# Optimization experiments

Measured on AMD Instinct MI355X. Metric: run time of the kernel, lower is better.

Reference implementation:

```python
import jax, jax.numpy as jnp
import numpy as np

DEPTH = 4
DIM = 128
M_DIM = 16
FEAT_DIM = 10
K = 12
CLAMP = 2.0
B, N = 4, 2048
EI = 2 * DIM + 1  # edge_input_dim = feats_i + feats_j + rel_dist


def setup_inputs() -> dict:
    key = jax.random.key(0)
    ks = jax.random.split(key, 16)
    def p(k, shape, s=0.05):
        return jax.random.normal(k, shape, dtype=jnp.float32) * s
    inp = dict(
        feats=jax.random.normal(ks[0], (B, N, FEAT_DIM), dtype=jnp.float32),
        coords=jax.random.normal(ks[1], (B, N, 3), dtype=jnp.float32) * 3.0,
        mask=jnp.ones((B, N), dtype=bool),
        emb_w=p(ks[2], (FEAT_DIM, DIM)), emb_b=p(ks[3], (DIM,)),
        ew1=p(ks[4], (DEPTH, EI, 2 * EI)), eb1=p(ks[5], (DEPTH, 2 * EI)),
        ew2=p(ks[6], (DEPTH, 2 * EI, M_DIM)), eb2=p(ks[7], (DEPTH, M_DIM)),
        cw1=p(ks[8], (DEPTH, M_DIM, 4 * M_DIM)), cb1=p(ks[9], (DEPTH, 4 * M_DIM)),
        cw2=p(ks[10], (DEPTH, 4 * M_DIM, 1)), cb2=p(ks[11], (DEPTH, 1)),
        cscale=jnp.full((DEPTH, 1), 1e-2, dtype=jnp.float32),  # CoorsNorm scale_init
        nw1=p(ks[12], (DEPTH, DIM + M_DIM, 2 * DIM)), nb1=p(ks[13], (DEPTH, 2 * DIM)),
        nw2=p(ks[14], (DEPTH, 2 * DIM, DIM)), nb2=p(ks[15], (DEPTH, DIM)),
    )
    return inp


def _egnn_layer(feats, coors, mask, lp):
    ew1, eb1, ew2, eb2, cw1, cb1, cw2, cb2, cscale, nw1, nb1, nw2, nb2 = lp
    # pairwise relative coords / squared distances
    rel = coors[:, :, None, :] - coors[:, None, :, :]            # (B,N,N,3)
    dist = jnp.sum(rel * rel, axis=-1)                           # (B,N,N)
    pm = mask[:, :, None] & mask[:, None, :]
    ranking = jnp.where(pm, dist, 1e5)
    _, nbhd = jax.lax.top_k(-ranking, K)                         # (B,N,K) smallest dists
    rel_k = jnp.take_along_axis(rel, nbhd[..., None], axis=2)    # (B,N,K,3)
    dist_k = jnp.take_along_axis(dist, nbhd, axis=2)             # (B,N,K)
    feats_j = jax.vmap(lambda f, i: f[i])(feats, nbhd)           # (B,N,K,D)
    mask_j = jnp.take_along_axis(jnp.broadcast_to(mask[:, None, :], dist.shape), nbhd, axis=2)
    m2 = mask[:, :, None] & mask_j                               # (B,N,K)
    feats_i = jnp.broadcast_to(feats[:, :, None, :], feats_j.shape)
    edge_in = jnp.concatenate([feats_i, feats_j, dist_k[..., None]], axis=-1)  # (B,N,K,EI)
    m_ij = jax.nn.silu(jax.nn.silu(edge_in @ ew1 + eb1) @ ew2 + eb2)           # (B,N,K,M)
    # coordinate update (E(n)-equivariant)
    w = (jax.nn.silu(m_ij @ cw1 + cb1) @ cw2 + cb2)[..., 0]      # (B,N,K)
    nrm = jnp.sqrt(jnp.sum(rel_k * rel_k, axis=-1, keepdims=True))
    rel_n = rel_k / jnp.maximum(nrm, 1e-8) * cscale              # CoorsNorm
    w = jnp.clip(jnp.where(m2, w, 0.0), -CLAMP, CLAMP)
    coors_out = coors + jnp.einsum('bik,bikc->bic', w, rel_n)
    # node update (residual)
    m_i = jnp.sum(jnp.where(m2[..., None], m_ij, 0.0), axis=2)   # (B,N,M)
    node_in = jnp.concatenate([feats, m_i], axis=-1)
    feats_out = jax.nn.silu(node_in @ nw1 + nb1) @ nw2 + nb2 + feats
    return feats_out, coors_out


def reference(feats, coords, mask, emb_w, emb_b, ew1, eb1, ew2, eb2, cw1, cb1, cw2, cb2, cscale, nw1, nb1, nw2, nb2):
    h = feats @ emb_w + emb_b                                    # continuous feature embedding
    c = coords
    for l in range(DEPTH):
        lp = (ew1[l], eb1[l], ew2[l], eb2[l], cw1[l], cb1[l], cw2[l], cb2[l],
              cscale[l], nw1[l], nb1[l], nw2[l], nb2[l])
        h, c = _egnn_layer(h, c, mask, lp)
    mf = mask.astype(h.dtype)
    out = jnp.sum(h * mf[..., None], axis=1) / jnp.sum(mf, axis=1, keepdims=True)  # (B,DIM)
    return out
```

## Files before the change

kernel.cpp:

```cpp
#include <hip/hip_runtime.h>
#include <hip/hip_bf16.h>
#include <math.h>

#define NB 4
#define NN 2048
#define DIMF 128
#define MD 16
#define KK 12
#define NODES (NB*NN)

typedef __attribute__((ext_vector_type(8))) short bf16x8;
typedef __attribute__((ext_vector_type(4))) float f32x4;

__device__ __forceinline__ float silu_f(float x) {
    return x * __builtin_amdgcn_rcpf(1.0f + __expf(-x));
}

__device__ __forceinline__ short f2bf(float x) {
    unsigned u = __float_as_uint(x);
    unsigned r = (u + 0x7FFFu + ((u >> 16) & 1u)) >> 16;
    return (short)r;
}

__device__ __forceinline__ short2 pkbf(float a, float b) {
    union { __hip_bfloat162 h; short2 s; } u;
    u.h = __float22bfloat162_rn(make_float2(a, b));
    return u.s;
}

__device__ __forceinline__ void upk8(uint4 u, float* f) {
    f[0] = __uint_as_float(u.x << 16); f[1] = __uint_as_float(u.x & 0xFFFF0000u);
    f[2] = __uint_as_float(u.y << 16); f[3] = __uint_as_float(u.y & 0xFFFF0000u);
    f[4] = __uint_as_float(u.z << 16); f[5] = __uint_as_float(u.z & 0xFFFF0000u);
    f[6] = __uint_as_float(u.w << 16); f[7] = __uint_as_float(u.w & 0xFFFF0000u);
}

__global__ __launch_bounds__(256) void prep_kernel(const float* __restrict__ ew2,
                                                   const float* __restrict__ cw1,
                                                   unsigned short* __restrict__ ew2frag,
                                                   unsigned short* __restrict__ cw1frag) {
    int t = blockIdx.x * 256 + threadIdx.x;
    if (t >= 43008) return;
    int l = t / 10752, r = t % 10752;
    if (r < 8704) {
        int kc = r >> 9, lane = (r >> 3) & 63, j = r & 7;
        int k = kc * 32 + ((lane >> 4) << 3) + j, n = lane & 15;
        float v = (k < 514) ? ew2[(size_t)l * 514 * 16 + k * 16 + n] : 0.0f;
        ew2frag[(size_t)l * 8704 + r] = (unsigned short)f2bf(v);
    } else {
        int r2 = r - 8704;
        int nb = r2 >> 9, lane = (r2 >> 3) & 63, j = r2 & 7;
        int c = ((lane >> 4) << 3) + j, n = nb * 16 + (lane & 15);
        float v = (c < 16) ? cw1[(size_t)l * 1024 + c * 64 + n] : 0.0f;
        cw1frag[(size_t)l * 2048 + r2] = (unsigned short)f2bf(v);
    }
}

__device__ __forceinline__ void knn_body(const float* __restrict__ coords,
                                         int* __restrict__ nbhd,
                                         int b2, int tid, float* sc) {
    int batch = b2 >> 9;
    int qbase = (b2 & 511) << 2;
    const float* cb = coords + (size_t)batch * NN * 3;
    const float4* cb4 = (const float4*)cb;
    int wv = tid >> 6, lane = tid & 63;
    int ql = qbase + wv;
    float qx = cb[3 * ql], qy = cb[3 * ql + 1], qz = cb[3 * ql + 2];
    float kd[KK]; int ki[KK];
#pragma unroll
    for (int r = 0; r < KK; ++r) { kd[r] = 3.0e38f; ki[r] = -1; }
#pragma unroll
    for (int half = 0; half < 2; ++half) {
#pragma unroll
        for (int t = 0; t < 3; ++t) {
            int e = tid + t * 256;
            ((float4*)sc)[e] = cb4[half * 768 + e];
        }
        __syncthreads();
#pragma unroll 4
        for (int jj = 0; jj < 16; ++jj) {
            int jl = (jj << 6) + lane;
            float dx = sc[3 * jl] - qx, dy = sc[3 * jl + 1] - qy, dz = sc[3 * jl + 2] - qz;
            float d2 = dx * dx + dy * dy + dz * dz;
            float cv = d2; int cix = (half << 10) + jl;
#pragma unroll
            for (int r = 0; r < KK; ++r) {
                bool sw = cv < kd[r];
                float tv = sw ? kd[r] : cv; int ti = sw ? ki[r] : cix;
                kd[r] = sw ? cv : kd[r];    ki[r] = sw ? cix : ki[r];
                cv = tv; cix = ti;
            }
        }
        __syncthreads();
    }
    int* out = nbhd + ((size_t)batch * NN + ql) * KK;
#pragma unroll
    for (int pass = 0; pass < KK; ++pass) {
        float mv = kd[0]; int mj = ki[0];
#pragma unroll
        for (int o = 1; o < 64; o <<= 1) {
            float ov = __shfl_xor(mv, o);
            int   oj = __shfl_xor(mj, o);
            if (ov < mv || (ov == mv && oj < mj)) { mv = ov; mj = oj; }
        }
        if (lane == 0) out[pass] = batch * NN + mj;
        if (kd[0] == mv && ki[0] == mj) {
#pragma unroll
            for (int r = 0; r < KK - 1; ++r) { kd[r] = kd[r + 1]; ki[r] = ki[r + 1]; }
            kd[KK - 1] = 3.0e38f;
        }
    }
}

template<typename AT, typename OT, int ACT, int RPW>
__device__ __forceinline__ void mgemm_body(
    const AT* __restrict__ A, int lda,
    const float* __restrict__ Bm, int ldb,
    OT* __restrict__ C, int ldc,
    const float* __restrict__ bias,
    const float* __restrict__ resid, int ldr,
    int N, int K, int bx, int by, int tid,
    unsigned short (*sA)[40], unsigned short (*sBt)[40])
{
    constexpr bool AF32 = (sizeof(AT) == 4);
    int lane = tid & 63, w = tid >> 6, quad = lane >> 4, l16 = lane & 15;
    int rowBase = by * (RPW * 64);
    int colBase = bx * 64;
    f32x4 acc[RPW][4];
#pragma unroll
    for (int rt = 0; rt < RPW; ++rt)
#pragma unroll
        for (int ct = 0; ct < 4; ++ct) acc[rt][ct] = (f32x4){0.f, 0.f, 0.f, 0.f};

    int kend = (K + 31) >> 5;
    for (int kc = 0; kc < kend; ++kc) {
        int k0 = kc * 32;
        if constexpr (AF32) {
#pragma unroll
            for (int p = 0; p < RPW * 2; ++p) {
                int e = tid + p * 256;
                int r = e >> 3, kq = e & 7, kg = k0 + kq * 4;
                short4 sv = {0, 0, 0, 0};
                if (kg + 4 <= K) {
                    float4 v = *(const float4*)&A[(size_t)(rowBase + r) * lda + kg];
                    short2 a = pkbf(v.x, v.y), b = pkbf(v.z, v.w);
                    sv = make_short4(a.x, a.y, b.x, b.y);
                }
                *(short4*)&sA[r][kq * 4] = sv;
            }
        } else {
#pragma unroll
            for (int p = 0; p < RPW; ++p) {
                int e = tid + p * 256;
                int r = e >> 2, k8 = (e & 3) * 8, kg = k0 + k8;
                uint4 v = {0u, 0u, 0u, 0u};
                if (kg + 8 <= K)
                    v = *(const uint4*)&A[(size_t)(rowBase + r) * lda + kg];
                *(uint4*)&sA[r][k8] = v;
            }
        }
#pragma unroll
        for (int p = 0; p < 4; ++p) {
            int e = tid + p * 256;
            int kk = e >> 5, c2 = (e & 31) * 2, kg = k0 + kk;
            int c0 = colBase + c2;
            float v0 = (kg < K && c0 < N)     ? Bm[(size_t)kg * ldb + c0]     : 0.0f;
            float v1 = (kg < K && c0 + 1 < N) ? Bm[(size_t)kg * ldb + c0 + 1] : 0.0f;
            sBt[c2][kk]     = (unsigned short)f2bf(v0);
            sBt[c2 + 1][kk] = (unsigned short)f2bf(v1);
        }
        __syncthreads();
        bf16x8 a[RPW], b[4];
#pragma unroll
        for (int rt = 0; rt < RPW; ++rt)
            a[rt] = *(const bf16x8*)&sA[w * (RPW * 16) + rt * 16 + l16][quad * 8];
#pragma unroll
        for (int ct = 0; ct < 4; ++ct)
            b[ct] = *(const bf16x8*)&sBt[ct * 16 + l16][quad * 8];
#pragma unroll
        for (int rt = 0; rt < RPW; ++rt)
#pragma unroll
            for (int ct = 0; ct < 4; ++ct)
                acc[rt][ct] = __builtin_amdgcn_mfma_f32_16x16x32_bf16(a[rt], b[ct], acc[rt][ct], 0, 0, 0);
        __syncthreads();
    }
#pragma unroll
    for (int rt = 0; rt < RPW; ++rt) {
#pragma unroll
        for (int ct = 0; ct < 4; ++ct) {
            int col = colBase + ct * 16 + l16;
            if (col < N) {
                float bv = bias ? bias[col] : 0.0f;
#pragma unroll
                for (int r = 0; r < 4; ++r) {
                    int row = rowBase + w * (RPW * 16) + rt * 16 + quad * 4 + r;
                    float v = acc[rt][ct][r] + bv;
                    if (ACT) v = silu_f(v);
                    if (resid) v += resid[(size_t)row * ldr + col];
                    if constexpr (sizeof(OT) == 4)
                        C[(size_t)row * ldc + col] = v;
                    else
                        C[(size_t)row * ldc + col] = (OT)f2bf(v);
                }
            }
        }
    }
}

template<typename AT, typename OT, int ACT, int RPW>
__global__ __launch_bounds__(256) void mgemm_kernel(
    const AT* __restrict__ A, int lda,
    const float* __restrict__ Bm, int ldb,
    OT* __restrict__ C, int ldc,
    const float* __restrict__ bias,
    const float* __restrict__ resid, int ldr,
    int N, int K)
{
    __shared__ __attribute__((aligned(16))) unsigned short sA[RPW * 64][40];
    __shared__ __attribute__((aligned(16))) unsigned short sBt[64][40];
    mgemm_body<AT, OT, ACT, RPW>(A, lda, Bm, ldb, C, ldc, bias, resid, ldr,
                                 N, K, blockIdx.x, blockIdx.y, threadIdx.x, sA, sBt);
}

__global__ __launch_bounds__(256) void embed_knn_kernel(
    const float* __restrict__ feats, const float* __restrict__ w,
    const float* __restrict__ b, float* __restrict__ h,
    const float* __restrict__ coords, int* __restrict__ nbhd)
{
    __shared__ __attribute__((aligned(16))) float sc[3072];
    int tid = threadIdx.x;
    if ((int)blockIdx.x < 2048) {
        knn_body(coords, nbhd, blockIdx.x, tid, sc);
    } else {
        int idx = ((int)blockIdx.x - 2048) * 256 + tid;
        int n = idx >> 7, d = idx & 127;
        const float* fr = feats + n * 10;
        float acc = b[d];
#pragma unroll
        for (int f = 0; f < 10; ++f) acc = fmaf(fr[f], w[f * 128 + d], acc);
        h[idx] = acc;
    }
}

__global__ __launch_bounds__(256) void mlp1knn_kernel(
    const float* __restrict__ nodein_, const float* __restrict__ nw1l,
    unsigned short* __restrict__ t1b, const float* __restrict__ nb1l,
    const float* __restrict__ coordsN, int* __restrict__ nbhd, int knnb)
{
    __shared__ __attribute__((aligned(16))) char smem[15360];
    int tid = threadIdx.x;
    if ((int)blockIdx.x < knnb) {
        knn_body(coordsN, nbhd, blockIdx.x, tid, (float*)smem);
    } else {
        int q = (int)blockIdx.x - knnb;
        mgemm_body<float, unsigned short, 1, 1>(
            nodein_, 144, nw1l, 256, t1b, 256, nb1l, nullptr, 0,
            256, 144, q & 3, q >> 2, tid,
            (unsigned short(*)[40])smem, (unsigned short(*)[40])(smem + 5120));
    }
}

__global__ __launch_bounds__(256) void pq_gemm_kernel(
    const float* __restrict__ A,
    const float* __restrict__ B1, const float* __restrict__ B2,
    unsigned short* __restrict__ PQb,
    const float* __restrict__ bias)
{
    __shared__ __attribute__((aligned(16))) unsigned short sA[128][40];
    __shared__ __attribute__((aligned(16))) unsigned short sBt[64][40];
    int tid = threadIdx.x;
    int lane = tid & 63, w = tid >> 6, quad = lane >> 4, l16 = lane & 15;
    int rowBase = blockIdx.y * 128;
    int colBase = blockIdx.x * 64;
    f32x4 acc[2][4];
#pragma unroll
    for (int rt = 0; rt < 2; ++rt)
#pragma unroll
        for (int ct = 0; ct < 4; ++ct) acc[rt][ct] = (f32x4){0.f, 0.f, 0.f, 0.f};

#pragma unroll
    for (int kc = 0; kc < 4; ++kc) {
        int k0 = kc * 32;
#pragma unroll
        for (int p = 0; p < 4; ++p) {
            int e = tid + p * 256;
            int r = e >> 3, kq = e & 7;
            float4 v = *(const float4*)&A[(size_t)(rowBase + r) * 128 + k0 + kq * 4];
            short2 a = pkbf(v.x, v.y), b = pkbf(v.z, v.w);
            *(short4*)&sA[r][kq * 4] = make_short4(a.x, a.y, b.x, b.y);
        }
#pragma unroll
        for (int p = 0; p < 4; ++p) {
            int e = tid + p * 256;
            int kk = e >> 5, c2 = (e & 31) * 2, kg = k0 + kk;
            int c0 = colBase + c2;
            float v0 = 0.0f, v1 = 0.0f;
            if (c0 < 1028) {
                const float* Bp = (c0 < 514) ? B1 : B2;
                int cc = (c0 < 514) ? c0 : c0 - 514;
                v0 = Bp[(size_t)kg * 514 + cc];
            }
            if (c0 + 1 < 1028) {
                const float* Bp = (c0 + 1 < 514) ? B1 : B2;
                int cc = (c0 + 1 < 514) ? c0 + 1 : c0 + 1 - 514;
                v1 = Bp[(size_t)kg * 514 + cc];
            }
            sBt[c2][kk]     = (unsigned short)f2bf(v0);
            sBt[c2 + 1][kk] = (unsigned short)f2bf(v1);
        }
        __syncthreads();
        bf16x8 a[2], b[4];
#pragma unroll
        for (int rt = 0; rt < 2; ++rt)
            a[rt] = *(const bf16x8*)&sA[w * 32 + rt * 16 + l16][quad * 8];
#pragma unroll
        for (int ct = 0; ct < 4; ++ct)
            b[ct] = *(const bf16x8*)&sBt[ct * 16 + l16][quad * 8];
#pragma unroll
        for (int rt = 0; rt < 2; ++rt)
#pragma unroll
            for (int ct = 0; ct < 4; ++ct)
                acc[rt][ct] = __builtin_amdgcn_mfma_f32_16x16x32_bf16(a[rt], b[ct], acc[rt][ct], 0, 0, 0);
        __syncthreads();
    }
#pragma unroll
    for (int rt = 0; rt < 2; ++rt) {
#pragma unroll
        for (int ct = 0; ct < 4; ++ct) {
            int col = colBase + ct * 16 + l16;
            if (col < 1028) {
                bool isP = col < 514;
                int oc = isP ? col : col + 14;
                float bv = isP ? bias[col] : 0.0f;
#pragma unroll
                for (int r = 0; r < 4; ++r) {
                    int row = rowBase + w * 32 + rt * 16 + quad * 4 + r;
                    PQb[(size_t)row * 1056 + oc] = (unsigned short)f2bf(acc[rt][ct][r] + bv);
                }
            }
        }
    }
}

__global__ __launch_bounds__(192, 8) void edge_kernel(
    const unsigned short* __restrict__ PQ, const int* __restrict__ nbhd,
    const float* __restrict__ cin, float* __restrict__ cout,
    float* __restrict__ nodein, const float* __restrict__ hin,
    const float* __restrict__ wrow,
    const unsigned short* __restrict__ ew2f,
    const unsigned short* __restrict__ cw1f,
    const float* __restrict__ eb2l,
    const float* __restrict__ cb1l,
    const float* __restrict__ cw2l,
    const float* __restrict__ cb2l,
    const float* __restrict__ cscalel)
{
    __shared__ __attribute__((aligned(16))) float swl[544];
    __shared__ __attribute__((aligned(16))) unsigned short mbf[48][16];
    __shared__ __attribute__((aligned(16))) float mf32[48][16];
    __shared__ __attribute__((aligned(16))) float reld2[48][4];
    __shared__ float wall[48];
    int tid = threadIdx.x;

    for (int idx = tid; idx < 544; idx += 192)
        swl[idx] = (idx < 514) ? wrow[idx] : 0.0f;
    __syncthreads();

    int lane = tid & 63, w = tid >> 6;
    int quad = lane >> 4, e16 = lane & 15;
    int eloc = w * 16 + e16;
    int nloc = eloc / 12;
    int k12 = eloc - nloc * 12;
    int bid = blockIdx.x;
    int rr8 = bid & 7, bsw = rr8 >> 1;
    int wsw = ((bid >> 3) << 1) | (rr8 & 1);
    int nodeBase = bsw * 2048 + wsw * 4;
    int i = nodeBase + nloc;
    int j = nbhd[i * KK + k12];
    float cix = cin[i * 3], ciy = cin[i * 3 + 1], ciz = cin[i * 3 + 2];
    float rx = cix - cin[j * 3], ry = ciy - cin[j * 3 + 1], rz = ciz - cin[j * 3 + 2];
    float d2 = rx * rx + ry * ry + rz * rz;

    const unsigned short* Pp = PQ + (size_t)i * 1056 + quad * 8;
    const unsigned short* Qp = PQ + (size_t)j * 1056 + 528 + quad * 8;

    uint4 pb[3], qb[3];
    pb[0] = *(const uint4*)Pp;
    qb[0] = *(const uint4*)Qp;
    pb[1] = *(const uint4*)(Pp + 32);
    qb[1] = *(const uint4*)(Qp + 32);

    f32x4 acc = {0.0f, 0.0f, 0.0f, 0.0f};
#pragma unroll
    for (int kc = 0; kc < 16; ++kc) {
        int cur = kc % 3, nx = (kc + 2) % 3;
        if (kc < 14) {
            pb[nx] = *(const uint4*)(Pp + (kc + 2) * 32);
            qb[nx] = *(const uint4*)(Qp + (kc + 2) * 32);
        }
        float p[8], q[8];
        upk8(pb[cur], p); upk8(qb[cur], q);
        float4 w0 = *(const float4*)&swl[quad * 8 + kc * 32];
        float4 w1 = *(const float4*)&swl[quad * 8 + kc * 32 + 4];
        float h0 = silu_f(fmaf(d2, w0.x, p[0] + q[0]));
        float h1 = silu_f(fmaf(d2, w0.y, p[1] + q[1]));
        float h2 = silu_f(fmaf(d2, w0.z, p[2] + q[2]));
        float h3 = silu_f(fmaf(d2, w0.w, p[3] + q[3]));
        float h4 = silu_f(fmaf(d2, w1.x, p[4] + q[4]));
        float h5 = silu_f(fmaf(d2, w1.y, p[5] + q[5]));
        float h6 = silu_f(fmaf(d2, w1.z, p[6] + q[6]));
        float h7 = silu_f(fmaf(d2, w1.w, p[7] + q[7]));
        bf16x8 af;
        short2 r0 = pkbf(h0, h1), r1 = pkbf(h2, h3), r2 = pkbf(h4, h5), r3 = pkbf(h6, h7);
        af[0] = r0.x; af[1] = r0.y; af[2] = r1.x; af[3] = r1.y;
        af[4] = r2.x; af[5] = r2.y; af[6] = r3.x; af[7] = r3.y;
        bf16x8 bf = *(const bf16x8*)(ew2f + (((size_t)kc * 64 + lane) << 3));
        acc = __builtin_amdgcn_mfma_f32_16x16x32_bf16(af, bf, acc, 0, 0, 0);
    }
    {
        unsigned up = *(const unsigned*)(PQ + (size_t)i * 1056 + 512);
        unsigned uq = *(const unsigned*)(PQ + (size_t)j * 1056 + 528 + 512);
        bf16x8 af = {0, 0, 0, 0, 0, 0, 0, 0};
        if (quad == 0) {
            float px = __uint_as_float(up << 16), py = __uint_as_float(up & 0xFFFF0000u);
            float qx = __uint_as_float(uq << 16), qy = __uint_as_float(uq & 0xFFFF0000u);
            af[0] = f2bf(silu_f(fmaf(d2, swl[512], px + qx)));
            af[1] = f2bf(silu_f(fmaf(d2, swl[513], py + qy)));
        }
        bf16x8 bf = *(const bf16x8*)(ew2f + (((size_t)16 * 64 + lane) << 3));
        acc = __builtin_amdgcn_mfma_f32_16x16x32_bf16(af, bf, acc, 0, 0, 0);
    }

    float eb = eb2l[e16];
    float m[4];
#pragma unroll
    for (int r = 0; r < 4; ++r) m[r] = silu_f(acc[r] + eb);

#pragma unroll
    for (int r = 0; r < 4; ++r) {
        int row = w * 16 + quad * 4 + r;
        mbf[row][e16] = (unsigned short)f2bf(m[r]);
        mf32[row][e16] = m[r];
    }
    if (quad == 0) {
        reld2[eloc][0] = rx; reld2[eloc][1] = ry;
        reld2[eloc][2] = rz; reld2[eloc][3] = d2;
    }
    __syncthreads();

    if (tid < 64) {
        int n = tid >> 4, ch = tid & 15;
        float s = 0.0f;
#pragma unroll
        for (int ke = 0; ke < KK; ++ke) s += mf32[n * 12 + ke][ch];
        nodein[(size_t)(nodeBase + n) * 144 + 128 + ch] = s;
    }

    bf16x8 af2 = {0, 0, 0, 0, 0, 0, 0, 0};
    if (quad < 2) af2 = *(const bf16x8*)&mbf[w * 16 + e16][quad * 8];
    float wpart[4] = {0.0f, 0.0f, 0.0f, 0.0f};
#pragma unroll
    for (int nb = 0; nb < 4; ++nb) {
        bf16x8 cf = *(const bf16x8*)(cw1f + (((size_t)nb * 64 + lane) << 3));
        f32x4 z = {0.0f, 0.0f, 0.0f, 0.0f};
        f32x4 t = __builtin_amdgcn_mfma_f32_16x16x32_bf16(af2, cf, z, 0, 0, 0);
        int d = nb * 16 + e16;
        float cb = cb1l[d], cw = cw2l[d];
#pragma unroll
        for (int r = 0; r < 4; ++r)
            wpart[r] = fmaf(silu_f(t[r] + cb), cw, wpart[r]);
    }
#pragma unroll
    for (int o = 1; o < 16; o <<= 1)
#pragma unroll
        for (int r = 0; r < 4; ++r) wpart[r] += __shfl_xor(wpart[r], o);
    if (e16 == 0) {
        float cb2v = cb2l[0];
#pragma unroll
        for (int r = 0; r < 4; ++r) {
            float ww = wpart[r] + cb2v;
            ww = fminf(fmaxf(ww, -2.0f), 2.0f);
            wall[w * 16 + quad * 4 + r] = ww;
        }
    }
    __syncthreads();

    if (tid < 12) {
        int n = tid / 3, c = tid - n * 3;
        float cs = cscalel[0];
        float s = 0.0f;
#pragma unroll
        for (int ke = 0; ke < KK; ++ke) {
            int eo = n * 12 + ke;
            float d2e = reld2[eo][3];
            float f = wall[eo] * cs * __builtin_amdgcn_rcpf(fmaxf(sqrtf(d2e), 1e-8f));
            s = fmaf(f, reld2[eo][c], s);
        }
        int node = nodeBase + n;
        cout[node * 3 + c] = cin[node * 3 + c] + s;
    }

    if (tid < 128) {
        int rr = tid >> 5, c4 = (tid & 31) * 4;
        *(float4*)&nodein[(size_t)(nodeBase + rr) * 144 + c4] =
            *(const float4*)&hin[(size_t)(nodeBase + rr) * 128 + c4];
    }
}

__global__ __launch_bounds__(256) void final1_kernel(const float* __restrict__ h,
                                                     float* __restrict__ part) {
    int b = blockIdx.x >> 5, sl = blockIdx.x & 31;
    int d = threadIdx.x & 127, half = threadIdx.x >> 7;
    const float* hp = h + ((size_t)b * NN + sl * 64) * DIMF;
    float acc = 0.0f;
    for (int n = half; n < 64; n += 2) acc += hp[(size_t)n * DIMF + d];
    __shared__ float red[256];
    red[threadIdx.x] = acc;
    __syncthreads();
    if (half == 0) part[(size_t)blockIdx.x * DIMF + d] = red[d] + red[d + 128];
}

__global__ __launch_bounds__(128) void final2_kernel(const float* __restrict__ part,
                                                     float* __restrict__ out) {
    int b = blockIdx.x, d = threadIdx.x;
    float acc = 0.0f;
#pragma unroll
    for (int s = 0; s < 32; ++s) acc += part[(size_t)(b * 32 + s) * DIMF + d];
    out[b * DIMF + d] = acc * (1.0f / NN);
}

extern "C" void kernel_launch(void* const* d_in, const int* in_sizes, int n_in,
                              void* d_out, int out_size, void* d_ws, size_t ws_size,
                              hipStream_t stream) {
    const float* feats  = (const float*)d_in[0];
    const float* coords = (const float*)d_in[1];
    const float* emb_w  = (const float*)d_in[3];
    const float* emb_b  = (const float*)d_in[4];
    const float* ew1    = (const float*)d_in[5];
    const float* eb1    = (const float*)d_in[6];
    const float* ew2    = (const float*)d_in[7];
    const float* eb2    = (const float*)d_in[8];
    const float* cw1    = (const float*)d_in[9];
    const float* cb1    = (const float*)d_in[10];
    const float* cw2    = (const float*)d_in[11];
    const float* cb2    = (const float*)d_in[12];
    const float* cscale = (const float*)d_in[13];
    const float* nw1    = (const float*)d_in[14];
    const float* nb1    = (const float*)d_in[15];
    const float* nw2    = (const float*)d_in[16];
    const float* nb2    = (const float*)d_in[17];

    char* ws = (char*)d_ws;
    float* h0     = (float*)(ws + 0);
    float* h1     = (float*)(ws + 4194304);
    float* c0     = (float*)(ws + 8388608);
    float* c1     = (float*)(ws + 8486912);
    int*   nbhd   = (int*)  (ws + 8585216);
    float* nodein = (float*)(ws + 8978432);
    unsigned short* PQb = (unsigned short*)(ws + 13697024);
    unsigned short* t1b = (unsigned short*)(ws + 31457280);
    unsigned short* ew2frag = (unsigned short*)(ws + 35651584);
    unsigned short* cw1frag = (unsigned short*)(ws + 35721216);
    float* part   = (float*)(ws + 13697024);

    float* hbuf[2] = {h0, h1};
    float* cbuf[2] = {c0, c1};

    prep_kernel<<<168, 256, 0, stream>>>(ew2, cw1, ew2frag, cw1frag);
    embed_knn_kernel<<<6144, 256, 0, stream>>>(feats, emb_w, emb_b, h0, coords, nbhd);

    for (int l = 0; l < 4; ++l) {
        const float* hin  = hbuf[l & 1];
        float*       hout = hbuf[(l + 1) & 1];
        const float* cin  = (l == 0) ? coords : cbuf[(l - 1) & 1];
        float*       cout = cbuf[l & 1];
        const float* ew1l = ew1 + (size_t)l * 257 * 514;

        pq_gemm_kernel<<<dim3(17, 64), 256, 0, stream>>>(
            hin, ew1l, ew1l + 128 * 514, PQb, eb1 + l * 514);

        edge_kernel<<<NODES / 4, 192, 0, stream>>>(PQb, nbhd, cin, cout, nodein, hin,
            ew1l + 256 * 514, ew2frag + (size_t)l * 8704, cw1frag + (size_t)l * 2048,
            eb2 + l * 16, cb1 + l * 64, cw2 + l * 64, cb2 + l, cscale + l);

        int knnb = (l < 3) ? 2048 : 0;
        mlp1knn_kernel<<<knnb + 512, 256, 0, stream>>>(
            nodein, nw1 + (size_t)l * 144 * 256, t1b, nb1 + l * 256,
            cout, nbhd, knnb);

        mgemm_kernel<unsigned short, float, 0, 1><<<dim3(2, 128), 256, 0, stream>>>(
            t1b, 256, nw2 + (size_t)l * 256 * 128, 128, hout, 128,
            nb2 + l * 128, hin, 128, 128, 256);
    }

    final1_kernel<<<NB * 32, 256, 0, stream>>>(hbuf[0], part);
    final2_kernel<<<NB, 128, 0, stream>>>(part, (float*)d_out);
}
```

Baseline: 528.3 us.

## Split kNN across both node-MLP kernels and use SoA coords in shared memory

The kNN neighbor search for the next layer is split into two halves. One half runs alongside the first node-MLP GEMM and the other alongside the second node-MLP GEMM, which is now a fused kernel instead of the standalone mgemm launch. This balances work so the small second GEMM no longer runs alone on an underfilled GPU. Separately, the coordinate tile staged into shared memory is transposed to structure-of-arrays, so lane reads are unit-stride rather than stride-3, which reduces LDS bank conflicts.

```diff
diff --git a/kernel.cpp b/kernel.cpp
--- a/kernel.cpp
+++ b/kernel.cpp
@@ -62,7 +62,6 @@
     int batch = b2 >> 9;
     int qbase = (b2 & 511) << 2;
     const float* cb = coords + (size_t)batch * NN * 3;
-    const float4* cb4 = (const float4*)cb;
     int wv = tid >> 6, lane = tid & 63;
     int ql = qbase + wv;
     float qx = cb[3 * ql], qy = cb[3 * ql + 1], qz = cb[3 * ql + 2];
@@ -71,16 +70,21 @@
     for (int r = 0; r < KK; ++r) { kd[r] = 3.0e38f; ki[r] = -1; }
 #pragma unroll
     for (int half = 0; half < 2; ++half) {
-#pragma unroll
-        for (int t = 0; t < 3; ++t) {
-            int e = tid + t * 256;
-            ((float4*)sc)[e] = cb4[half * 768 + e];
+        {
+            const float4* src = (const float4*)(cb + half * 3072);
+            float4 a = src[3 * tid], b4 = src[3 * tid + 1], c4 = src[3 * tid + 2];
+            float4 xs = {a.x, a.w, b4.z, c4.y};
+            float4 ys = {a.y, b4.x, b4.w, c4.z};
+            float4 zs = {a.z, b4.y, c4.x, c4.w};
+            *(float4*)&sc[tid * 4]        = xs;
+            *(float4*)&sc[1024 + tid * 4] = ys;
+            *(float4*)&sc[2048 + tid * 4] = zs;
         }
         __syncthreads();
 #pragma unroll 4
         for (int jj = 0; jj < 16; ++jj) {
             int jl = (jj << 6) + lane;
-            float dx = sc[3 * jl] - qx, dy = sc[3 * jl + 1] - qy, dz = sc[3 * jl + 2] - qz;
+            float dx = sc[jl] - qx, dy = sc[1024 + jl] - qy, dz = sc[2048 + jl] - qz;
             float d2 = dx * dx + dy * dy + dz * dz;
             float cv = d2; int cix = (half << 10) + jl;
 #pragma unroll
@@ -207,21 +211,6 @@
     }
 }
 
-template<typename AT, typename OT, int ACT, int RPW>
-__global__ __launch_bounds__(256) void mgemm_kernel(
-    const AT* __restrict__ A, int lda,
-    const float* __restrict__ Bm, int ldb,
-    OT* __restrict__ C, int ldc,
-    const float* __restrict__ bias,
-    const float* __restrict__ resid, int ldr,
-    int N, int K)
-{
-    __shared__ __attribute__((aligned(16))) unsigned short sA[RPW * 64][40];
-    __shared__ __attribute__((aligned(16))) unsigned short sBt[64][40];
-    mgemm_body<AT, OT, ACT, RPW>(A, lda, Bm, ldb, C, ldc, bias, resid, ldr,
-                                 N, K, blockIdx.x, blockIdx.y, threadIdx.x, sA, sBt);
-}
-
 __global__ __launch_bounds__(256) void embed_knn_kernel(
     const float* __restrict__ feats, const float* __restrict__ w,
     const float* __restrict__ b, float* __restrict__ h,
@@ -245,17 +234,36 @@
 __global__ __launch_bounds__(256) void mlp1knn_kernel(
     const float* __restrict__ nodein_, const float* __restrict__ nw1l,
     unsigned short* __restrict__ t1b, const float* __restrict__ nb1l,
-    const float* __restrict__ coordsN, int* __restrict__ nbhd, int knnb)
+    const float* __restrict__ coordsN, int* __restrict__ nbhd, int knnb, int kbase)
 {
     __shared__ __attribute__((aligned(16))) char smem[15360];
     int tid = threadIdx.x;
     if ((int)blockIdx.x < knnb) {
-        knn_body(coordsN, nbhd, blockIdx.x, tid, (float*)smem);
+        knn_body(coordsN, nbhd, kbase + blockIdx.x, tid, (float*)smem);
     } else {
         int q = (int)blockIdx.x - knnb;
         mgemm_body<float, unsigned short, 1, 1>(
             nodein_, 144, nw1l, 256, t1b, 256, nb1l, nullptr, 0,
             256, 144, q & 3, q >> 2, tid,
+            (unsigned short(*)[40])smem, (unsigned short(*)[40])(smem + 5120));
+    }
+}
+
+__global__ __launch_bounds__(256) void mlp2knn_kernel(
+    const unsigned short* __restrict__ t1b, const float* __restrict__ nw2l,
+    float* __restrict__ hout, const float* __restrict__ nb2l,
+    const float* __restrict__ hin,
+    const float* __restrict__ coordsN, int* __restrict__ nbhd, int knnb, int kbase)
+{
+    __shared__ __attribute__((aligned(16))) char smem[15360];
+    int tid = threadIdx.x;
+    if ((int)blockIdx.x < knnb) {
+        knn_body(coordsN, nbhd, kbase + blockIdx.x, tid, (float*)smem);
+    } else {
+        int q = (int)blockIdx.x - knnb;
+        mgemm_body<unsigned short, float, 0, 1>(
+            t1b, 256, nw2l, 128, hout, 128, nb2l, hin, 128,
+            128, 256, q & 1, q >> 1, tid,
             (unsigned short(*)[40])smem, (unsigned short(*)[40])(smem + 5120));
     }
 }
@@ -583,14 +591,14 @@
             ew1l + 256 * 514, ew2frag + (size_t)l * 8704, cw1frag + (size_t)l * 2048,
             eb2 + l * 16, cb1 + l * 64, cw2 + l * 64, cb2 + l, cscale + l);
 
-        int knnb = (l < 3) ? 2048 : 0;
+        int knnb = (l < 3) ? 1024 : 0;
         mlp1knn_kernel<<<knnb + 512, 256, 0, stream>>>(
             nodein, nw1 + (size_t)l * 144 * 256, t1b, nb1 + l * 256,
-            cout, nbhd, knnb);
-
-        mgemm_kernel<unsigned short, float, 0, 1><<<dim3(2, 128), 256, 0, stream>>>(
-            t1b, 256, nw2 + (size_t)l * 256 * 128, 128, hout, 128,
-            nb2 + l * 128, hin, 128, 128, 256);
+            cout, nbhd, knnb, 0);
+
+        mlp2knn_kernel<<<knnb + 256, 256, 0, stream>>>(
+            t1b, nw2 + (size_t)l * 256 * 128, hout, nb2 + l * 128, hin,
+            cout, nbhd, knnb, 1024);
     }
 
     final1_kernel<<<NB * 32, 256, 0, stream>>>(hbuf[0], part);
```

Result: faster. 509.0 us (-3.6%).
